# Kernel optimization log

Hardware: AMD Instinct MI355X
Metric: run time of the kernel (lower is better)

Reference implementation:

```python
import math
import jax, jax.numpy as jnp
import numpy as np

B, C, T, N, H = 4, 512, 2048, 4096, 4


def setup_inputs() -> dict:
    key = jax.random.key(0)
    ks = jax.random.split(key, 6)
    w = lambda k, shape: jax.random.normal(k, shape, dtype=jnp.float32) * 0.02
    return {
        "hidden_states": jax.random.normal(ks[0], (B, C, T), dtype=jnp.float32),
        "codebook_hidden_states": jax.random.normal(ks[1], (N, C), dtype=jnp.float32),
        # Linear weights stored as (in, out) so application is x @ W + b
        "Wq": w(ks[2], (C, C)), "bq": jnp.zeros((C,), jnp.float32),
        "Wk": w(ks[3], (C, C)), "bk": jnp.zeros((C,), jnp.float32),
        "Wv": w(ks[4], (C, C)), "bv": jnp.zeros((C,), jnp.float32),
        "Wp": w(ks[5], (C, H)), "bp": jnp.zeros((H,), jnp.float32),
    }


def reference(hidden_states, codebook_hidden_states, Wq, bq, Wk, bk, Wv, bv, Wp, bp):
    b, c, t = hidden_states.shape
    n = codebook_hidden_states.shape[0]
    h = bp.shape[0]
    d = c // h
    hs = hidden_states.transpose(0, 2, 1)                               # [B,T,C]
    q = (hs @ Wq + bq).reshape(b, t, h, d).transpose(0, 2, 1, 3)        # [B,H,T,d]
    k = (codebook_hidden_states @ Wk + bk).reshape(n, h, d).transpose(1, 0, 2)  # [H,N,d]
    v = codebook_hidden_states @ Wv + bv                                # [N,C]
    cg = hs @ Wp + bp                                                   # [B,T,H] head-pool gates
    scale = 1.0 / math.sqrt(d)
    logits_h = jnp.einsum('bhtd,hnd->bhnt', q, k) * scale               # [B,H,N,T]
    logits = jnp.einsum('bth,bhnt->bnt', cg, logits_h) / math.sqrt(h)   # [B,N,T]
    soft = jax.nn.softmax(logits, axis=1)                               # over codebook axis N
    idx = jnp.argmax(soft, axis=1)                                      # [B,T]
    hard = jax.nn.one_hot(idx, n, dtype=logits.dtype).transpose(0, 2, 1)  # [B,N,T]
    # straight-through: value == hard, gradient flows through soft
    one_hot = soft + jax.lax.stop_gradient(hard - soft)
    z_q = jnp.einsum('bnt,nd->bdt', one_hot, v)                         # [B,C,T]
    return logits, idx[:, None, :], z_q
```

## Files before the change

### kernel.cpp

```cpp
#include <hip/hip_runtime.h>
#include <hip/hip_bf16.h>
#include <cstddef>
#include <cstdint>

#define BB 4
#define CC 512
#define TT 2048
#define NN 4096
#define HH 4

constexpr float KFAC       = 0.04419417382415922f;
constexpr float INV_S18    = 1.0f / 262144.0f;
constexpr float INV_SCALE2 = 1.0f / (512.0f * 512.0f);

typedef _Float16 f16x8 __attribute__((ext_vector_type(8)));
typedef _Float16 f16x4 __attribute__((ext_vector_type(4)));
typedef float    f32x4 __attribute__((ext_vector_type(4)));

__device__ __forceinline__ void gld16(const void* g, void* s) {
    __builtin_amdgcn_global_load_lds(
        (const __attribute__((address_space(1))) void*)g,
        (__attribute__((address_space(3))) void*)s, 16, 0, 0);
}

struct HL { _Float16 h, l; };
__device__ __forceinline__ HL split512(float x) {
    float v = x * 512.0f;
    _Float16 h = (_Float16)v;
    return { h, (_Float16)(v - (float)h) };
}

__global__ __launch_bounds__(256) void k_split(
    const float* __restrict__ src, _Float16* __restrict__ hi, _Float16* __restrict__ lo, int n4)
{
    int q = blockIdx.x * 256 + threadIdx.x;
    if (q >= n4) return;
    float4 v = *(const float4*)(src + (size_t)q * 4);
    f16x4 H, L;
    HL a = split512(v.x); H[0] = a.h; L[0] = a.l;
    HL b = split512(v.y); H[1] = b.h; L[1] = b.l;
    HL c = split512(v.z); H[2] = c.h; L[2] = c.l;
    HL d = split512(v.w); H[3] = d.h; L[3] = d.l;
    *(f16x4*)(hi + (size_t)q * 4) = H;
    *(f16x4*)(lo + (size_t)q * 4) = L;
}

__device__ __forceinline__ void tsplit_body(
    const float* __restrict__ src, _Float16* __restrict__ hi, _Float16* __restrict__ lo,
    int S, int R, int r0, int s0)
{
    __shared__ float ls[64][65];
    const int tid = threadIdx.x;
    #pragma unroll
    for (int i = 0; i < 4; ++i) {
        int q = tid + i * 256;
        int row = q >> 4, c4 = (q & 15) * 4;
        float4 v = *(const float4*)(src + (size_t)(r0 + row) * S + s0 + c4);
        ls[row][c4] = v.x; ls[row][c4 + 1] = v.y;
        ls[row][c4 + 2] = v.z; ls[row][c4 + 3] = v.w;
    }
    __syncthreads();
    #pragma unroll
    for (int i = 0; i < 2; ++i) {
        int q = tid + i * 256;
        int orow = q >> 3, seg = (q & 7) * 8;
        f16x8 H, L;
        #pragma unroll
        for (int j = 0; j < 8; ++j) {
            HL s = split512(ls[seg + j][orow]);
            H[j] = s.h; L[j] = s.l;
        }
        size_t off = (size_t)(s0 + orow) * R + r0 + seg;
        *(f16x8*)(hi + off) = H;
        *(f16x8*)(lo + off) = L;
    }
}

__global__ __launch_bounds__(256) void k_tsplit(
    const float* __restrict__ src, _Float16* __restrict__ hi, _Float16* __restrict__ lo,
    long sbatch, long dbatch, int S, int R)
{
    src += (size_t)blockIdx.z * sbatch;
    hi  += (size_t)blockIdx.z * dbatch;
    lo  += (size_t)blockIdx.z * dbatch;
    tsplit_body(src, hi, lo, S, R, blockIdx.y * 64, blockIdx.x * 64);
}

__global__ __launch_bounds__(256) void k_tsplit_w(
    const float* __restrict__ w0, const float* __restrict__ w1, const float* __restrict__ w2,
    _Float16* __restrict__ h0, _Float16* __restrict__ h1, _Float16* __restrict__ h2,
    _Float16* __restrict__ l0, _Float16* __restrict__ l1, _Float16* __restrict__ l2)
{
    const int z = blockIdx.z;
    const float* src = z == 0 ? w0 : z == 1 ? w1 : w2;
    _Float16* hi = z == 0 ? h0 : z == 1 ? h1 : h2;
    _Float16* lo = z == 0 ? l0 : z == 1 ? l1 : l2;
    tsplit_body(src, hi, lo, CC, CC, blockIdx.y * 64, blockIdx.x * 64);
}

#define MFMA_TILE_DECLS                                                       \
    __shared__ __align__(16) _Float16 Ah[128][32];                            \
    __shared__ __align__(16) _Float16 Al[128][32];                            \
    __shared__ __align__(16) _Float16 Bh[128][32];                            \
    __shared__ __align__(16) _Float16 Bl[128][32];                            \
    const int tid  = threadIdx.x;                                             \
    const int w    = tid >> 6;                                                \
    const int l    = tid & 63;                                                \
    const int quad = l >> 4;                                                  \
    const int l15  = l & 15;                                                  \
    const int wm   = (w >> 1) * 64;                                           \
    const int wn   = (w & 1) * 64;                                            \
    const int rA   = l >> 2;                                                  \
    const int cA   = (l & 3) * 8;                                             \
    f32x4 acc[4][4];                                                          \
    _Pragma("unroll") for (int i = 0; i < 4; ++i)                             \
        _Pragma("unroll") for (int j = 0; j < 4; ++j)                         \
            acc[i][j] = (f32x4){0.f, 0.f, 0.f, 0.f};

#define MFMA_TILE_STAGE(pAh, pAl, pBh, pBl, k0, srcStride)                    \
    gld16(pAh + k0,                    &Ah[w * 32][0]);                       \
    gld16(pAh + k0 + 16 * (srcStride), &Ah[w * 32 + 16][0]);                  \
    gld16(pAl + k0,                    &Al[w * 32][0]);                       \
    gld16(pAl + k0 + 16 * (srcStride), &Al[w * 32 + 16][0]);                  \
    gld16(pBh + k0,                    &Bh[w * 32][0]);                       \
    gld16(pBh + k0 + 16 * (srcStride), &Bh[w * 32 + 16][0]);                  \
    gld16(pBl + k0,                    &Bl[w * 32][0]);                       \
    gld16(pBl + k0 + 16 * (srcStride), &Bl[w * 32 + 16][0]);

#define MFMA_TILE_COMPUTE                                                     \
    {                                                                         \
        f16x8 fah[4], fal[4], fbh[4], fbl[4];                                 \
        _Pragma("unroll") for (int i = 0; i < 4; ++i) {                       \
            fah[i] = *(const f16x8*)&Ah[wm + i * 16 + l15][quad * 8];         \
            fal[i] = *(const f16x8*)&Al[wm + i * 16 + l15][quad * 8];         \
            fbh[i] = *(const f16x8*)&Bh[wn + i * 16 + l15][quad * 8];         \
            fbl[i] = *(const f16x8*)&Bl[wn + i * 16 + l15][quad * 8];         \
        }                                                                     \
        _Pragma("unroll") for (int i = 0; i < 4; ++i)                         \
            _Pragma("unroll") for (int j = 0; j < 4; ++j) {                   \
                acc[i][j] = __builtin_amdgcn_mfma_f32_16x16x32_f16(fah[i], fbh[j], acc[i][j], 0, 0, 0); \
                acc[i][j] = __builtin_amdgcn_mfma_f32_16x16x32_f16(fah[i], fbl[j], acc[i][j], 0, 0, 0); \
                acc[i][j] = __builtin_amdgcn_mfma_f32_16x16x32_f16(fal[i], fbh[j], acc[i][j], 0, 0, 0); \
            }                                                                 \
    }

__global__ __launch_bounds__(256, 2) void k_proj_all(
    const _Float16* __restrict__ hsTh, const _Float16* __restrict__ hsTl,
    const _Float16* __restrict__ cbhi, const _Float16* __restrict__ cblo,
    const _Float16* __restrict__ wqTh, const _Float16* __restrict__ wqTl,
    const _Float16* __restrict__ wkTh, const _Float16* __restrict__ wkTl,
    const _Float16* __restrict__ wvTh, const _Float16* __restrict__ wvTl,
    const float* __restrict__ bq, const float* __restrict__ bk, const float* __restrict__ bv,
    const float* __restrict__ Wp, const float* __restrict__ bp,
    _Float16* __restrict__ qhi, _Float16* __restrict__ qlo,
    _Float16* __restrict__ khi, _Float16* __restrict__ klo, float* __restrict__ vproj)
{
    const int z    = blockIdx.z;
    const int y    = blockIdx.y;
    const int c0   = blockIdx.x * 128;
    const int path = z == 0 ? 0 : (y < 32 ? 1 : 2);
    const int m0   = (z == 0 ? y : (y & 31)) * 128;
    const int hblk = c0 >> 7;

    const _Float16* srcAh = z == 0 ? hsTh : cbhi;
    const _Float16* srcAl = z == 0 ? hsTl : cblo;
    const _Float16* bTh   = path == 0 ? wqTh : path == 1 ? wkTh : wvTh;
    const _Float16* bTl   = path == 0 ? wqTl : path == 1 ? wkTl : wvTl;
    const float*    bias  = path == 0 ? bq   : path == 1 ? bk   : bv;

    MFMA_TILE_DECLS
    __shared__ float wp_sh[32];
    __shared__ float gate_sh[128];
    float gate = 0.f;

    const _Float16* pAh = srcAh + (size_t)(m0 + w * 32 + rA) * CC + cA;
    const _Float16* pAl = srcAl + (size_t)(m0 + w * 32 + rA) * CC + cA;
    const _Float16* pBh = bTh   + (size_t)(c0 + w * 32 + rA) * CC + cA;
    const _Float16* pBl = bTl   + (size_t)(c0 + w * 32 + rA) * CC + cA;

    for (int k0 = 0; k0 < CC; k0 += 32) {
        MFMA_TILE_STAGE(pAh, pAl, pBh, pBl, k0, CC)
        if (path == 0 && tid < 32) wp_sh[tid] = Wp[(size_t)(k0 + tid) * HH + hblk];
        __syncthreads();
        MFMA_TILE_COMPUTE
        if (path == 0 && tid < 128) {
            #pragma unroll
            for (int s = 0; s < 4; ++s) {
                f16x8 hv = *(const f16x8*)&Ah[tid][s * 8];
                f16x8 lv = *(const f16x8*)&Al[tid][s * 8];
                #pragma unroll
                for (int jj = 0; jj < 8; ++jj)
                    gate = fmaf((float)hv[jj] + (float)lv[jj], wp_sh[s * 8 + jj], gate);
            }
        }
        __syncthreads();
    }

    if (path == 0) {
        if (tid < 128)
            gate_sh[tid] = (gate * (1.0f / 512.0f) + bp[hblk]) * KFAC;
        __syncthreads();
        #pragma unroll
        for (int i = 0; i < 4; ++i)
            #pragma unroll
            for (int j = 0; j < 4; ++j) {
                int col = c0 + wn + j * 16 + l15;
                float bi = bias[col];
                #pragma unroll
                for (int r = 0; r < 4; ++r) {
                    int rloc = wm + i * 16 + quad * 4 + r;
                    float v = fmaf(acc[i][j][r], INV_S18, bi) * gate_sh[rloc];
                    HL s = split512(v);
                    qhi[(size_t)(m0 + rloc) * CC + col] = s.h;
                    qlo[(size_t)(m0 + rloc) * CC + col] = s.l;
                }
            }
    } else if (path == 1) {
        #pragma unroll
        for (int i = 0; i < 4; ++i)
            #pragma unroll
            for (int j = 0; j < 4; ++j) {
                int col = c0 + wn + j * 16 + l15;
                float bi = bias[col];
                #pragma unroll
                for (int r = 0; r < 4; ++r) {
                    int row = m0 + wm + i * 16 + quad * 4 + r;
                    float v = fmaf(acc[i][j][r], INV_S18, bi);
                    HL s = split512(v);
                    khi[(size_t)row * CC + col] = s.h;
                    klo[(size_t)row * CC + col] = s.l;
                }
            }
    } else {
        #pragma unroll
        for (int i = 0; i < 4; ++i)
            #pragma unroll
            for (int j = 0; j < 4; ++j) {
                int col = c0 + wn + j * 16 + l15;
                float bi = bias[col];
                #pragma unroll
                for (int r = 0; r < 4; ++r) {
                    int row = m0 + wm + i * 16 + quad * 4 + r;
                    vproj[(size_t)row * CC + col] = fmaf(acc[i][j][r], INV_S18, bi);
                }
            }
    }
}

#define BAR   __builtin_amdgcn_s_barrier()
#define LGKM0 { asm volatile("s_waitcnt lgkmcnt(0)" ::: "memory"); __builtin_amdgcn_sched_barrier(0); }
#define PRIO1 __builtin_amdgcn_s_setprio(1)
#define PRIO0 __builtin_amdgcn_s_setprio(0)
#define VMW(N) asm volatile("s_waitcnt vmcnt(" #N ")" ::: "memory")

#define ST_A3(BUF, SRC) {                                                     \
    gld16((SRC) + lsrc,           &smem[(BUF) * 16384 + w * 512]);            \
    gld16((SRC) + lsrc + 64 * CC, &smem[(BUF) * 16384 + 4096 + w * 512]);     \
}
#define ST_B3(BUF, SRC) {                                                     \
    gld16((SRC) + lsrc,           &smem[(BUF) * 16384 + 8192 + w * 512]);     \
    gld16((SRC) + lsrc + 64 * CC, &smem[(BUF) * 16384 + 12288 + w * 512]);    \
}
#define RD_A3(BUF, H) {                                                       \
    _Pragma("unroll") for (int ii = 0; ii < 4; ++ii)                          \
        ah[ii] = *(const f16x8*)&smem[(BUF) * 16384 + ((H) * 4 + ii) * 1024 + baseRdA]; \
}
#define RD_B3(BUF) {                                                          \
    _Pragma("unroll") for (int jj = 0; jj < 4; ++jj)                          \
        bf[jj] = *(const f16x8*)&smem[(BUF) * 16384 + baseRdB + jj * 1024];   \
}
#define MM3(IOFF) {                                                           \
    _Pragma("unroll") for (int ii = 0; ii < 4; ++ii)                          \
        _Pragma("unroll") for (int jj = 0; jj < 4; ++jj)                      \
            acc[(IOFF) + ii][jj] = __builtin_amdgcn_mfma_f32_16x16x32_f16(    \
                ah[ii], bf[jj], acc[(IOFF) + ii][jj], 0, 0, 0);               \
}
#define TILE3(BUF, SBUF, AS, BS, DOST, VW) {                                  \
    if (DOST) ST_A3(SBUF, AS);                                                \
    RD_A3(BUF, 0); RD_B3(BUF);                                                \
    BAR; LGKM0; PRIO1; MM3(0); PRIO0; BAR;                                    \
    if (DOST) ST_B3(SBUF, BS);                                                \
    RD_A3(BUF, 1);                                                            \
    BAR; LGKM0; PRIO1; MM3(4); PRIO0; VW; BAR;                                \
}
#define APTR(n) ((((n) >> 4) == 1 ? klo : khi) + arow0 + ((n) & 15) * 32)
#define BPTR(n) ((((n) >> 4) == 2 ? qlo : qhi) + brow0 + ((n) & 15) * 32)

__global__ __launch_bounds__(512, 2) void k_logits_8p(
    const _Float16* __restrict__ khi, const _Float16* __restrict__ klo,
    const _Float16* __restrict__ qhi, const _Float16* __restrict__ qlo,
    float* __restrict__ logits,
    float* __restrict__ pval,
    int*   __restrict__ pidx)
{
    __shared__ __align__(16) _Float16 smem[65536];

    const int f  = blockIdx.x + 8 * (blockIdx.y + 16 * blockIdx.z);
    const int fs = (f & 7) * 64 + (f >> 3);
    const int t0 = (fs & 7) * 256;
    const int by = (fs >> 3) & 15;
    const int b  = fs >> 7;
    const int n0 = by * 256;

    const int tid  = threadIdx.x;
    const int w    = tid >> 6;
    const int l    = tid & 63;
    const int quad = l >> 4;
    const int l15  = l & 15;
    const int wm   = (w >> 2) * 128;
    const int ha   = w >> 2;
    const int wn   = (w & 3) * 64;

    const size_t arow0 = (size_t)n0 * CC;
    const size_t brow0 = ((size_t)b * TT + t0) * CC;

    const int    lclog = (l & 7) ^ ((l >> 3) & 7);
    const size_t lsrc  = (size_t)(w * 8 + (l >> 3) + (lclog >> 2) * 128) * CC
                       + (size_t)(lclog & 3) * 8;

    const int cpxA    = ((ha << 2) | quad) ^ (l15 & 7);
    const int baseRdA = l15 * 64 + cpxA * 8;
    const int cpxB    = ((((w & 3) >> 1) << 2) | quad) ^ (l15 & 7);
    const int baseRdB = 8192 + (w & 1) * 4096 + l15 * 64 + cpxB * 8;

    f32x4 acc[8][4];
    #pragma unroll
    for (int i = 0; i < 8; ++i)
        #pragma unroll
        for (int j = 0; j < 4; ++j)
            acc[i][j] = (f32x4){0.f, 0.f, 0.f, 0.f};
    f16x8 ah[4];
    f16x8 bf[4];

    ST_A3(0, APTR(0)); ST_B3(0, BPTR(0));
    ST_A3(1, APTR(1)); ST_B3(1, BPTR(1));
    ST_A3(2, APTR(2)); ST_B3(2, BPTR(2));
    VMW(8); BAR;

    #pragma unroll 1
    for (int g = 0; g < 11; ++g) {
        const int kt = g * 4;
        { const int n_ = kt + 3; const _Float16* as_ = APTR(n_); const _Float16* bs_ = BPTR(n_);
          TILE3(0, 3, as_, bs_, 1, VMW(8)); }
        { const int n_ = kt + 4; const _Float16* as_ = APTR(n_); const _Float16* bs_ = BPTR(n_);
          TILE3(1, 0, as_, bs_, 1, VMW(8)); }
        { const int n_ = kt + 5; const _Float16* as_ = APTR(n_); const _Float16* bs_ = BPTR(n_);
          TILE3(2, 1, as_, bs_, 1, VMW(8)); }
        { const int n_ = kt + 6; const _Float16* as_ = APTR(n_); const _Float16* bs_ = BPTR(n_);
          TILE3(3, 2, as_, bs_, 1, VMW(8)); }
    }
    { const _Float16* as_ = APTR(47); const _Float16* bs_ = BPTR(47);
      TILE3(0, 3, as_, bs_, 1, VMW(8)); }
    TILE3(1, 0, khi, khi, 0, VMW(4));
    TILE3(2, 0, khi, khi, 0, VMW(0));
    TILE3(3, 0, khi, khi, 0, (void)0);

    {
        const size_t lb = ((size_t)b * NN + n0 + wm) * TT + t0 + wn;
        #pragma unroll
        for (int i = 0; i < 8; ++i)
            #pragma unroll
            for (int r = 0; r < 4; ++r) {
                const size_t rowoff = lb + (size_t)(i * 16 + quad * 4 + r) * TT;
                #pragma unroll
                for (int j = 0; j < 4; ++j)
                    logits[rowoff + j * 16 + l15] = acc[i][j][r] * INV_SCALE2;
            }
    }
    float bvj[4]; int bnj[4];
    #pragma unroll
    for (int j = 0; j < 4; ++j) {
        float bv = -3.0e38f; int bn = 0;
        #pragma unroll
        for (int i = 0; i < 8; ++i)
            #pragma unroll
            for (int r = 0; r < 4; ++r) {
                float v = acc[i][j][r] * INV_SCALE2;
                int row = n0 + wm + i * 16 + quad * 4 + r;
                if (v > bv) { bv = v; bn = row; }
            }
        #pragma unroll
        for (int m = 16; m <= 32; m <<= 1) {
            float ov = __shfl_xor(bv, m, 64);
            int   on = __shfl_xor(bn, m, 64);
            if (ov > bv || (ov == bv && on < bn)) { bv = ov; bn = on; }
        }
        bvj[j] = bv; bnj[j] = bn;
    }
    float* rv = (float*)smem;
    int*   ri = (int*)(smem + 1024);
    __syncthreads();
    if (w >= 4 && l < 16) {
        #pragma unroll
        for (int j = 0; j < 4; ++j) {
            rv[wn + j * 16 + l] = bvj[j];
            ri[wn + j * 16 + l] = bnj[j];
        }
    }
    __syncthreads();
    if (w < 4 && l < 16) {
        #pragma unroll
        for (int j = 0; j < 4; ++j) {
            int cl = wn + j * 16 + l;
            float bv = bvj[j]; int bn = bnj[j];
            float ov = rv[cl];
            if (ov > bv) { bv = ov; bn = ri[cl]; }
            size_t o = ((size_t)b * 16 + by) * TT + t0 + cl;
            pval[o] = bv;
            pidx[o] = bn;
        }
    }
}

__global__ __launch_bounds__(256) void k_finalize(
    const float* __restrict__ pval,
    const int*   __restrict__ pidx,
    const float* __restrict__ vproj,
    float* __restrict__ idx_out,
    float* __restrict__ zq)
{
    const int b  = blockIdx.y;
    const int t0 = blockIdx.x * 32;
    const int tid = threadIdx.x;

    __shared__ int sfin[32];
    if (tid < 32) {
        const int t = t0 + tid;
        float bv = -3.0e38f; int bn = 0;
        #pragma unroll
        for (int k = 0; k < 16; ++k) {
            size_t o = ((size_t)b * 16 + k) * TT + t;
            float v = pval[o];
            if (v > bv) { bv = v; bn = pidx[o]; }
        }
        idx_out[(size_t)b * TT + t] = (float)bn;
        sfin[tid] = bn;
    }
    __syncthreads();
    for (int pos = tid; pos < 32 * CC; pos += 256) {
        int c = pos >> 5, tl = pos & 31;
        zq[((size_t)b * CC + c) * TT + t0 + tl] = vproj[(size_t)sfin[tl] * CC + c];
    }
}

extern "C" void kernel_launch(void* const* d_in, const int* in_sizes, int n_in,
                              void* d_out, int out_size, void* d_ws, size_t ws_size,
                              hipStream_t stream)
{
    (void)in_sizes; (void)n_in; (void)out_size; (void)ws_size;
    const float* hs = (const float*)d_in[0];
    const float* cb = (const float*)d_in[1];
    const float* Wq = (const float*)d_in[2];
    const float* bq = (const float*)d_in[3];
    const float* Wk = (const float*)d_in[4];
    const float* bk = (const float*)d_in[5];
    const float* Wv = (const float*)d_in[6];
    const float* bv = (const float*)d_in[7];
    const float* Wp = (const float*)d_in[8];
    const float* bp = (const float*)d_in[9];

    char* ws = (char*)d_ws;
    const size_t MB = 1024 * 1024;
    _Float16* hsTh = (_Float16*)(ws);
    _Float16* hsTl = (_Float16*)(ws + 8  * MB);
    _Float16* qhi  = (_Float16*)(ws + 16 * MB);
    _Float16* qlo  = (_Float16*)(ws + 24 * MB);
    _Float16* cbhi = (_Float16*)(ws + 32 * MB);
    _Float16* cblo = (_Float16*)(ws + 36 * MB);
    _Float16* khi  = (_Float16*)(ws + 40 * MB);
    _Float16* klo  = (_Float16*)(ws + 44 * MB);
    float*    vproj= (float*)   (ws + 48 * MB);
    _Float16* wqTh = (_Float16*)(ws + 56 * MB);
    _Float16* wqTl = (_Float16*)(ws + 56 * MB + 524288);
    _Float16* wkTh = (_Float16*)(ws + 57 * MB);
    _Float16* wkTl = (_Float16*)(ws + 57 * MB + 524288);
    _Float16* wvTh = (_Float16*)(ws + 58 * MB);
    _Float16* wvTl = (_Float16*)(ws + 58 * MB + 524288);
    float* pval = (float*)(ws + 32 * MB);
    int*   pidx = (int*)  (ws + 33 * MB);

    float* logits = (float*)d_out;
    float* idxf   = logits + (size_t)BB * NN * TT;
    float* zq     = idxf + (size_t)BB * TT;

    k_split<<<dim3((NN * CC / 4 + 255) / 256), 256, 0, stream>>>(
        cb, cbhi, cblo, NN * CC / 4);
    k_tsplit<<<dim3(TT / 64, CC / 64, BB), 256, 0, stream>>>(
        hs, hsTh, hsTl, (long)CC * TT, (long)TT * CC, TT, CC);
    k_tsplit_w<<<dim3(CC / 64, CC / 64, 3), 256, 0, stream>>>(
        Wq, Wk, Wv, wqTh, wkTh, wvTh, wqTl, wkTl, wvTl);

    k_proj_all<<<dim3(CC / 128, 64, 2), 256, 0, stream>>>(
        hsTh, hsTl, cbhi, cblo,
        wqTh, wqTl, wkTh, wkTl, wvTh, wvTl,
        bq, bk, bv, Wp, bp,
        qhi, qlo, khi, klo, vproj);

    k_logits_8p<<<dim3(TT / 256, NN / 256, BB), 512, 0, stream>>>(
        khi, klo, qhi, qlo, logits, pval, pidx);

    k_finalize<<<dim3(TT / 32, BB), 256, 0, stream>>>(
        pval, pidx, vproj, idxf, zq);
}
```

Baseline: 335.8 us.

## Software-pipeline LDS fragment reads across tiles with double-buffered B registers

Restructures the GEMM main loop so each tile's LDS-to-register reads for the next tile (B fragments and even A half) are issued before the current tile's MFMAs. It uses ping-pong register buffers and drops the explicit lgkmcnt(0) waits. It also tightens the vmcnt waits from 8 to 4 to match the new ordering. The goal is to hide LDS read latency behind MFMA work. The cost is more live registers at an occupancy target of 2 waves per SIMD, plus a tail that must be handled by hand.

```diff
diff --git a/kernel.cpp b/kernel.cpp
--- a/kernel.cpp
+++ b/kernel.cpp
@@ -248,7 +248,7 @@
 }
 
 #define BAR   __builtin_amdgcn_s_barrier()
-#define LGKM0 { asm volatile("s_waitcnt lgkmcnt(0)" ::: "memory"); __builtin_amdgcn_sched_barrier(0); }
+#define SB0   __builtin_amdgcn_sched_barrier(0)
 #define PRIO1 __builtin_amdgcn_s_setprio(1)
 #define PRIO0 __builtin_amdgcn_s_setprio(0)
 #define VMW(N) asm volatile("s_waitcnt vmcnt(" #N ")" ::: "memory")
@@ -261,27 +261,37 @@
     gld16((SRC) + lsrc,           &smem[(BUF) * 16384 + 8192 + w * 512]);     \
     gld16((SRC) + lsrc + 64 * CC, &smem[(BUF) * 16384 + 12288 + w * 512]);    \
 }
-#define RD_A3(BUF, H) {                                                       \
+#define RD_AE(BUF) {                                                          \
     _Pragma("unroll") for (int ii = 0; ii < 4; ++ii)                          \
-        ah[ii] = *(const f16x8*)&smem[(BUF) * 16384 + ((H) * 4 + ii) * 1024 + baseRdA]; \
-}
-#define RD_B3(BUF) {                                                          \
-    _Pragma("unroll") for (int jj = 0; jj < 4; ++jj)                          \
-        bf[jj] = *(const f16x8*)&smem[(BUF) * 16384 + baseRdB + jj * 1024];   \
-}
-#define MM3(IOFF) {                                                           \
+        aE[ii] = *(const f16x8*)&smem[(BUF) * 16384 + ii * 1024 + baseRdA];   \
+}
+#define RD_AO(BUF) {                                                          \
+    _Pragma("unroll") for (int ii = 0; ii < 4; ++ii)                          \
+        aO[ii] = *(const f16x8*)&smem[(BUF) * 16384 + (4 + ii) * 1024 + baseRdA]; \
+}
+#define RD_BP(BUF, P, DST) {                                                  \
+    DST[(P) * 2]     = *(const f16x8*)&smem[(BUF) * 16384 + baseRdB + ((P) * 2) * 1024];     \
+    DST[(P) * 2 + 1] = *(const f16x8*)&smem[(BUF) * 16384 + baseRdB + ((P) * 2 + 1) * 1024]; \
+}
+#define MM_H(IOFF, A, B) {                                                    \
     _Pragma("unroll") for (int ii = 0; ii < 4; ++ii)                          \
         _Pragma("unroll") for (int jj = 0; jj < 4; ++jj)                      \
             acc[(IOFF) + ii][jj] = __builtin_amdgcn_mfma_f32_16x16x32_f16(    \
-                ah[ii], bf[jj], acc[(IOFF) + ii][jj], 0, 0, 0);               \
-}
-#define TILE3(BUF, SBUF, AS, BS, DOST, VW) {                                  \
+                (A)[ii], (B)[jj], acc[(IOFF) + ii][jj], 0, 0, 0);             \
+}
+#define TILE_P(BUF, NBUF, SBUF, AS, BS, CUR, NXT, DOST, VME) {                \
+    RD_BP(NBUF, 0, NXT);                                                      \
     if (DOST) ST_A3(SBUF, AS);                                                \
-    RD_A3(BUF, 0); RD_B3(BUF);                                                \
-    BAR; LGKM0; PRIO1; MM3(0); PRIO0; BAR;                                    \
+    RD_AO(BUF);                                                               \
+    SB0; BAR;                                                                 \
+    PRIO1; MM_H(0, aE, CUR); PRIO0;                                           \
+    BAR;                                                                      \
     if (DOST) ST_B3(SBUF, BS);                                                \
-    RD_A3(BUF, 1);                                                            \
-    BAR; LGKM0; PRIO1; MM3(4); PRIO0; VW; BAR;                                \
+    RD_BP(NBUF, 1, NXT);                                                      \
+    RD_AE(NBUF);                                                              \
+    SB0; BAR;                                                                 \
+    PRIO1; MM_H(4, aO, CUR); PRIO0;                                           \
+    VME; BAR;                                                                 \
 }
 #define APTR(n) ((((n) >> 4) == 1 ? klo : khi) + arow0 + ((n) & 15) * 32)
 #define BPTR(n) ((((n) >> 4) == 2 ? qlo : qhi) + brow0 + ((n) & 15) * 32)
@@ -329,31 +339,36 @@
         #pragma unroll
         for (int j = 0; j < 4; ++j)
             acc[i][j] = (f32x4){0.f, 0.f, 0.f, 0.f};
-    f16x8 ah[4];
-    f16x8 bf[4];
+    f16x8 aE[4], aO[4];
+    f16x8 bb0[4], bb1[4];
 
     ST_A3(0, APTR(0)); ST_B3(0, BPTR(0));
     ST_A3(1, APTR(1)); ST_B3(1, BPTR(1));
     ST_A3(2, APTR(2)); ST_B3(2, BPTR(2));
-    VMW(8); BAR;
+    VMW(4); BAR;
+    RD_AE(0); RD_BP(0, 0, bb0); RD_BP(0, 1, bb0);
 
     #pragma unroll 1
     for (int g = 0; g < 11; ++g) {
         const int kt = g * 4;
-        { const int n_ = kt + 3; const _Float16* as_ = APTR(n_); const _Float16* bs_ = BPTR(n_);
-          TILE3(0, 3, as_, bs_, 1, VMW(8)); }
-        { const int n_ = kt + 4; const _Float16* as_ = APTR(n_); const _Float16* bs_ = BPTR(n_);
-          TILE3(1, 0, as_, bs_, 1, VMW(8)); }
-        { const int n_ = kt + 5; const _Float16* as_ = APTR(n_); const _Float16* bs_ = BPTR(n_);
-          TILE3(2, 1, as_, bs_, 1, VMW(8)); }
-        { const int n_ = kt + 6; const _Float16* as_ = APTR(n_); const _Float16* bs_ = BPTR(n_);
-          TILE3(3, 2, as_, bs_, 1, VMW(8)); }
+        { const _Float16* as_ = APTR(kt + 3); const _Float16* bs_ = BPTR(kt + 3);
+          TILE_P(0, 1, 3, as_, bs_, bb0, bb1, 1, VMW(4)); }
+        { const _Float16* as_ = APTR(kt + 4); const _Float16* bs_ = BPTR(kt + 4);
+          TILE_P(1, 2, 0, as_, bs_, bb1, bb0, 1, VMW(4)); }
+        { const _Float16* as_ = APTR(kt + 5); const _Float16* bs_ = BPTR(kt + 5);
+          TILE_P(2, 3, 1, as_, bs_, bb0, bb1, 1, VMW(4)); }
+        { const _Float16* as_ = APTR(kt + 6); const _Float16* bs_ = BPTR(kt + 6);
+          TILE_P(3, 0, 2, as_, bs_, bb1, bb0, 1, VMW(4)); }
     }
     { const _Float16* as_ = APTR(47); const _Float16* bs_ = BPTR(47);
-      TILE3(0, 3, as_, bs_, 1, VMW(8)); }
-    TILE3(1, 0, khi, khi, 0, VMW(4));
-    TILE3(2, 0, khi, khi, 0, VMW(0));
-    TILE3(3, 0, khi, khi, 0, (void)0);
+      TILE_P(0, 1, 3, as_, bs_, bb0, bb1, 1, VMW(4)); }
+    TILE_P(1, 2, 0, khi, khi, bb1, bb0, 0, VMW(0));
+    TILE_P(2, 3, 1, khi, khi, bb0, bb1, 0, (void)0);
+    RD_AO(3);
+    SB0; BAR;
+    PRIO1; MM_H(0, aE, bb1); PRIO0;
+    BAR;
+    PRIO1; MM_H(4, aO, bb1); PRIO0;
 
     {
         const size_t lb = ((size_t)b * NN + n0 + wm) * TT + t0 + wn;
```

New measurement: 332.6 us. About the same (-1.0%).
